# Performance work log

Hardware: AMD Instinct MI355X
Metric: run time of the kernel (lower is better)

Reference implementation:

```python
import jax, jax.numpy as jnp
import numpy as np

B, C, N, M = 4, 256, 4096, 4096
H, D = 4, 64  # num_heads, head_dim = C // H


def _proj(x, W, b):
    # Conv1d(kernel_size=1): pointwise linear over channel dim. x:(B,Cin,L) W:(Cout,Cin) b:(Cout,)
    return jnp.einsum('oc,bcn->bon', W, x) + b[None, :, None]


def setup_inputs() -> dict:
    key = jax.random.key(0)
    ks = jax.random.split(key, 10)
    s = 1.0 / np.sqrt(C)
    return {
        'query': jax.random.normal(ks[0], (B, C, N), dtype=jnp.float32),
        'source': jax.random.normal(ks[1], (B, C, M), dtype=jnp.float32),
        'Wq': jax.random.normal(ks[2], (C, C), dtype=jnp.float32) * s,
        'bq': jnp.zeros((C,), dtype=jnp.float32),
        'Wk': jax.random.normal(ks[3], (C, C), dtype=jnp.float32) * s,
        'bk': jnp.zeros((C,), dtype=jnp.float32),
        'Wv': jax.random.normal(ks[4], (C, C), dtype=jnp.float32) * s,
        'bv': jnp.zeros((C,), dtype=jnp.float32),
        'Wm': jax.random.normal(ks[5], (C, C), dtype=jnp.float32) * s,
        'bm': jnp.zeros((C,), dtype=jnp.float32),
    }


def reference(query, source, Wq, bq, Wk, bk, Wv, bv, Wm, bm):
    b = query.shape[0]
    n = query.shape[-1]
    Q = _proj(query, Wq, bq).reshape(b, H, D, -1)   # (B,H,D,N)
    K = _proj(source, Wk, bk).reshape(b, H, D, -1)  # (B,H,D,M)
    V = _proj(source, Wv, bv).reshape(b, H, D, -1)  # (B,H,D,M)
    scores = jnp.einsum('bhdn,bhdm->bhnm', Q, K) / (D ** 0.5)
    attn = jax.nn.softmax(scores, axis=-1)
    out = jnp.einsum('bhnm,bhdm->bhdn', attn, V)    # (B,H,D,N)
    out = out.reshape(b, H * D, n)                   # (B,C,N)
    return _proj(out, Wm, bm)
```

## Files before the change

kernel.cpp:

```cpp
#include <hip/hip_runtime.h>
#include <hip/hip_bf16.h>
#include <stdint.h>

#define BB 4
#define CCH 256
#define NN 4096
#define MM 4096
#define HH 4
#define DDIM 64

typedef __attribute__((ext_vector_type(8))) short short8v;
typedef __attribute__((ext_vector_type(4))) float f32x4;
typedef __attribute__((ext_vector_type(16))) float f32x16;

__device__ __forceinline__ unsigned short f2b(float f) {
    unsigned int u = __builtin_bit_cast(unsigned int, f);
    unsigned int r = (u + 0x7FFFu + ((u >> 16) & 1u)) >> 16;
    return (unsigned short)r;
}

__device__ __forceinline__ f32x16 zero16() {
    f32x16 z;
#pragma unroll
    for (int i = 0; i < 16; i++) z[i] = 0.f;
    return z;
}

__global__ __launch_bounds__(256) void convert_kernel(
    const float* __restrict__ q, const float* __restrict__ s,
    const float* __restrict__ Wq, const float* __restrict__ Wk,
    const float* __restrict__ Wv, const float* __restrict__ Wm,
    unsigned short* __restrict__ XTq, unsigned short* __restrict__ XTs,
    unsigned short* __restrict__ Wb) {
    __shared__ float tile[64][65];
    const int bid = blockIdx.x, tid = threadIdx.x;
    if (bid < 2048) {
        const float* in = (bid < 1024) ? q : s;
        unsigned short* out = (bid < 1024) ? XTq : XTs;
        const int r = bid & 1023;
        const int b = r >> 8;
        const int rr = r & 255;
        const int l0 = (rr >> 2) * 64, c0 = (rr & 3) * 64;
#pragma unroll
        for (int i = 0; i < 16; i++) {
            int idx = tid + (i << 8);
            int cc = idx >> 6, ll = idx & 63;
            tile[cc][ll] = in[(size_t)(b * CCH + c0 + cc) * 4096 + l0 + ll];
        }
        __syncthreads();
#pragma unroll
        for (int i = 0; i < 16; i++) {
            int idx = tid + (i << 8);
            int ll = idx >> 6, cc = idx & 63;
            out[((size_t)(b * 4096 + l0 + ll) << 8) + c0 + cc] = f2b(tile[cc][ll]);
        }
    } else {
        const int wid = bid - 2048;
        const int wsel = wid >> 4;
        const float* src = (wsel == 0) ? Wq : (wsel == 1) ? Wk : (wsel == 2) ? Wv : Wm;
        const int off = (wid & 15) * 4096;
#pragma unroll
        for (int i = 0; i < 16; i++) {
            int idx = off + tid + (i << 8);
            Wb[(size_t)wsel * 65536 + idx] = f2b(src[idx]);
        }
    }
}

template <int OUTMODE, bool AHEAD>
__device__ __forceinline__ void gemm_body(const unsigned short* __restrict__ XT,
                                          const unsigned short* __restrict__ W,
                                          const float* __restrict__ bias,
                                          void* __restrict__ outv, float oscale) {
    constexpr int WSTR = 264;
    constexpr int XSTR = 40;
    __shared__ __align__(16) unsigned short Wlds[64 * WSTR];
    __shared__ __align__(16) unsigned short Xlds[256 * XSTR];
    const int tid = threadIdx.x, w = tid >> 6, l = tid & 63;
    const int lg = l >> 4, lm = l & 15;
    const int n0 = blockIdx.x * 256, o0 = blockIdx.y * 64;
    const int oh = (w >> 1) * 32, nh = (w & 1) * 128;

#pragma unroll
    for (int i = 0; i < 8; i++) {
        int idx = tid + (i << 8);
        int row = idx >> 5, c8 = (idx & 31) * 8;
        *(uint4*)&Wlds[row * WSTR + c8] = *(const uint4*)&W[(size_t)(o0 + row) * 256 + c8];
    }

    f32x4 acc[8][2];
#pragma unroll
    for (int nt = 0; nt < 8; nt++)
#pragma unroll
        for (int ot = 0; ot < 2; ot++) acc[nt][ot] = (f32x4){0.f, 0.f, 0.f, 0.f};

    for (int kc = 0; kc < 8; kc++) {
#pragma unroll
        for (int i = 0; i < 4; i++) {
            int idx = tid + (i << 8);
            int row = idx >> 2;
            const unsigned short* srcp;
            if constexpr (AHEAD) {
                int c = kc * 32 + (idx & 3) * 8;
                srcp = XT + ((size_t)(c >> 6) * 4096 + n0 + row) * 64 + (c & 63);
            } else {
                srcp = XT + (size_t)(n0 + row) * 256 + kc * 32 + (idx & 3) * 8;
            }
            *(uint4*)&Xlds[row * XSTR + (idx & 3) * 8] = *(const uint4*)srcp;
        }
        __syncthreads();
        short8v bfrag[2];
#pragma unroll
        for (int ot = 0; ot < 2; ot++)
            bfrag[ot] = *(const short8v*)&Wlds[(oh + ot * 16 + lm) * WSTR + kc * 32 + lg * 8];
#pragma unroll
        for (int nt = 0; nt < 8; nt++) {
            short8v af = *(const short8v*)&Xlds[(nh + nt * 16 + lm) * XSTR + lg * 8];
            acc[nt][0] = __builtin_amdgcn_mfma_f32_16x16x32_bf16(af, bfrag[0], acc[nt][0], 0, 0, 0);
            acc[nt][1] = __builtin_amdgcn_mfma_f32_16x16x32_bf16(af, bfrag[1], acc[nt][1], 0, 0, 0);
        }
        __syncthreads();
    }

#pragma unroll
    for (int nt = 0; nt < 8; nt++)
#pragma unroll
        for (int ot = 0; ot < 2; ot++) {
            int o = o0 + oh + ot * 16 + lm;
            int nb = n0 + nh + nt * 16 + lg * 4;
            float bb = bias[o];
            if constexpr (OUTMODE == 2) {
                float* out = (float*)outv;
                float4 v = make_float4(acc[nt][ot][0] + bb, acc[nt][ot][1] + bb,
                                       acc[nt][ot][2] + bb, acc[nt][ot][3] + bb);
                *(float4*)&out[(size_t)o * 4096 + nb] = v;
            } else if constexpr (OUTMODE == 0) {
                unsigned short* out = (unsigned short*)outv;
                __align__(8) unsigned short v[4];
#pragma unroll
                for (int t = 0; t < 4; t++) v[t] = f2b(acc[nt][ot][t] + bb);
                *(uint2*)&out[(size_t)o * 4096 + nb] = *(uint2*)v;
            } else {
                unsigned short* out = (unsigned short*)outv;
                unsigned short* outp = out + ((size_t)(o >> 6) * 4096 + nb) * 64 + (o & 63);
#pragma unroll
                for (int t = 0; t < 4; t++) outp[t * 64] = f2b((acc[nt][ot][t] + bb) * oscale);
            }
        }
}

__global__ __launch_bounds__(256) void gemm_qkv_kernel(
    const unsigned short* __restrict__ XTq, const unsigned short* __restrict__ XTs,
    const unsigned short* __restrict__ Wb,
    const float* __restrict__ bq, const float* __restrict__ bk, const float* __restrict__ bv,
    unsigned short* __restrict__ QT, unsigned short* __restrict__ KT,
    unsigned short* __restrict__ Vn) {
    const int z = blockIdx.z;
    const int b = z / 3, p = z - b * 3;
    const unsigned short* XT = ((p == 0) ? XTq : XTs) + (size_t)b * 4096 * 256;
    const unsigned short* W = Wb + p * 65536;
    const float* bias = (p == 0) ? bq : (p == 1) ? bk : bv;
    if (p == 2) {
        gemm_body<0, false>(XT, W, bias, Vn + (size_t)b * 256 * 4096, 1.0f);
    } else {
        unsigned short* out = ((p == 0) ? QT : KT) + (size_t)b * 1048576;
        gemm_body<1, false>(XT, W, bias, out, (p == 0) ? 0.1803368801f : 1.0f);
    }
}

__global__ __launch_bounds__(256) void gemm_final_kernel(
    const unsigned short* __restrict__ OH, const unsigned short* __restrict__ Wm,
    const float* __restrict__ bm, float* __restrict__ out) {
    const int b = blockIdx.z;
    gemm_body<2, true>(OH + (size_t)b * 1048576, Wm, bm, out + (size_t)b * 256 * 4096, 1.0f);
}

__device__ __forceinline__ void stage_kv(const unsigned short* __restrict__ Kb,
                                         const unsigned short* __restrict__ Vb,
                                         char* dst, int m0s, int tid) {
#pragma unroll
    for (int i = 0; i < 2; i++) {
        int ch = tid + (i << 8);
        int rr = ch >> 3, pp = ch & 7;
        int sw = (pp ^ (rr & 7)) << 4;
        const char* sK = (const char*)(Kb + ((size_t)(m0s + rr) << 6)) + sw;
        const char* sV = (const char*)(Vb + (size_t)rr * 4096 + m0s) + sw;
        __builtin_amdgcn_global_load_lds(
            (const __attribute__((address_space(1))) unsigned int*)sK,
            (__attribute__((address_space(3))) unsigned int*)(dst + (ch << 4)), 16, 0, 0);
        __builtin_amdgcn_global_load_lds(
            (const __attribute__((address_space(1))) unsigned int*)sV,
            (__attribute__((address_space(3))) unsigned int*)(dst + 8192 + (ch << 4)), 16, 0, 0);
    }
}

__global__ __launch_bounds__(256, 2) void attn_kernel(
    const unsigned short* __restrict__ QT, const unsigned short* __restrict__ KT,
    const unsigned short* __restrict__ Vn, unsigned short* __restrict__ OH) {
    __shared__ __align__(16) char smem[32768];
    const int tid = threadIdx.x, w = tid >> 6, l = tid & 63;
    const int lo5 = l & 31, hi = l >> 5;
    const int bh = blockIdx.y, b = bh >> 2, h = bh & 3;
    const int q0 = blockIdx.x * 128 + w * 32;

    short8v qf[4];
    {
        size_t qrow = ((size_t)bh * 4096 + q0 + lo5) * 64;
#pragma unroll
        for (int c = 0; c < 4; c++)
            qf[c] = *(const short8v*)&QT[qrow + c * 16 + hi * 8];
    }

    short8v ones;
#pragma unroll
    for (int j = 0; j < 8; j++) ones[j] = (short)0x3F80;
    f32x16 minit;
#pragma unroll
    for (int r = 0; r < 16; r++) minit[r] = -16.0f;

    const unsigned short* Vb = Vn + ((size_t)b * 256 + h * 64) * 4096;
    const unsigned short* Kb = KT + (size_t)bh * 262144;

    f32x16 o[2];
    o[0] = zero16();
    o[1] = zero16();
    f32x16 sacc = zero16();

    stage_kv(Kb, Vb, smem, 0, tid);

    for (int it = 0; it < 64; it++) {
        __syncthreads();
        char* cur = smem + ((it & 1) << 14);
        if (it < 63) stage_kv(Kb, Vb, smem + (((it + 1) & 1) << 14), (it + 1) * 64, tid);

        short8v kf[2][4];
#pragma unroll
        for (int mc = 0; mc < 2; mc++) {
            int m = mc * 32 + lo5;
#pragma unroll
            for (int c = 0; c < 4; c++)
                kf[mc][c] = *(const short8v*)(cur + m * 128 + (((c * 2 + hi) * 16) ^ ((m & 7) << 4)));
        }
        short8v vf[2][4];
#pragma unroll
        for (int dc = 0; dc < 2; dc++) {
            int d = dc * 32 + lo5;
#pragma unroll
            for (int c = 0; c < 4; c++)
                vf[dc][c] = *(const short8v*)(cur + 8192 + d * 128 + (((c * 2 + hi) * 16) ^ ((d & 7) << 4)));
        }

        f32x16 s[2];
#pragma unroll
        for (int mc = 0; mc < 2; mc++) {
            f32x16 a = __builtin_amdgcn_mfma_f32_32x32x16_bf16(kf[mc][0], qf[0], minit, 0, 0, 0);
#pragma unroll
            for (int c = 1; c < 4; c++)
                a = __builtin_amdgcn_mfma_f32_32x32x16_bf16(kf[mc][c], qf[c], a, 0, 0, 0);
            s[mc] = a;
        }

        short8v pv[2][2];
#pragma unroll
        for (int mc = 0; mc < 2; mc++) {
            float p[16];
#pragma unroll
            for (int r = 0; r < 16; r++) p[r] = exp2f(s[mc][r]);
#pragma unroll
            for (int half = 0; half < 2; half++) {
                union { unsigned int u[4]; short8v v; } pu;
#pragma unroll
                for (int wdx = 0; wdx < 2; wdx++) {
                    unsigned int a, bq;
                    asm("v_cvt_pk_bf16_f32 %0, %1, %2"
                        : "=v"(a) : "v"(p[half * 8 + 2 * wdx]), "v"(p[half * 8 + 2 * wdx + 1]));
                    asm("v_cvt_pk_bf16_f32 %0, %1, %2"
                        : "=v"(bq) : "v"(p[half * 8 + 4 + 2 * wdx]), "v"(p[half * 8 + 4 + 2 * wdx + 1]));
                    asm volatile("v_permlane32_swap_b32 %0, %1" : "+v"(a), "+v"(bq));
                    pu.u[wdx] = a;
                    pu.u[wdx + 2] = bq;
                }
                pv[mc][half] = pu.v;
            }
        }

#pragma unroll
        for (int mc = 0; mc < 2; mc++)
#pragma unroll
            for (int half = 0; half < 2; half++)
                sacc = __builtin_amdgcn_mfma_f32_32x32x16_bf16(ones, pv[mc][half], sacc, 0, 0, 0);

#pragma unroll
        for (int dc = 0; dc < 2; dc++)
#pragma unroll
            for (int mc = 0; mc < 2; mc++)
#pragma unroll
                for (int half = 0; half < 2; half++)
                    o[dc] = __builtin_amdgcn_mfma_f32_32x32x16_bf16(
                        vf[dc][2 * mc + half], pv[mc][half], o[dc], 0, 0, 0);
    }

    float inv = 1.f / sacc[0];
    __syncthreads();
    {
        int row = w * 32 + lo5;
        char* rbase = smem + row * 128;
        int sw = (row & 7) << 4;
#pragma unroll
        for (int dc = 0; dc < 2; dc++)
#pragma unroll
            for (int g = 0; g < 4; g++) {
                ushort4 v4;
                v4.x = f2b(o[dc][g * 4 + 0] * inv);
                v4.y = f2b(o[dc][g * 4 + 1] * inv);
                v4.z = f2b(o[dc][g * 4 + 2] * inv);
                v4.w = f2b(o[dc][g * 4 + 3] * inv);
                int colb = dc * 64 + g * 16 + hi * 8;
                *(ushort4*)(rbase + (colb ^ sw)) = v4;
            }
    }
    __syncthreads();
    {
        int row = tid >> 1, seg = (tid & 1) * 64;
        size_t gbase = ((size_t)bh * 4096 + blockIdx.x * 128 + row) * 64 + (size_t)(tid & 1) * 32;
        int sw = (row & 7) << 4;
#pragma unroll
        for (int ch = 0; ch < 4; ch++) {
            uint4 v = *(const uint4*)(smem + row * 128 + ((seg + ch * 16) ^ sw));
            *(uint4*)&OH[gbase + ch * 8] = v;
        }
    }
}

extern "C" void kernel_launch(void* const* d_in, const int* in_sizes, int n_in,
                              void* d_out, int out_size, void* d_ws, size_t ws_size,
                              hipStream_t stream) {
    const float* q  = (const float*)d_in[0];
    const float* s  = (const float*)d_in[1];
    const float* Wq = (const float*)d_in[2];
    const float* bq = (const float*)d_in[3];
    const float* Wk = (const float*)d_in[4];
    const float* bk = (const float*)d_in[5];
    const float* Wv = (const float*)d_in[6];
    const float* bv = (const float*)d_in[7];
    const float* Wm = (const float*)d_in[8];
    const float* bm = (const float*)d_in[9];
    float* out = (float*)d_out;
    char* ws = (char*)d_ws;

    const size_t SZ = (size_t)BB * 4096 * 256 * 2;
    unsigned short* XTq  = (unsigned short*)(ws);
    unsigned short* XTs  = (unsigned short*)(ws + SZ);
    unsigned short* Wb   = (unsigned short*)(ws + 2 * SZ);
    unsigned short* QT   = (unsigned short*)(ws + 2 * SZ + 524288);
    unsigned short* KTh  = (unsigned short*)(ws + 3 * SZ + 524288);
    unsigned short* Vnat = (unsigned short*)(ws + 4 * SZ + 524288);
    unsigned short* OH   = XTq;

    convert_kernel<<<2112, 256, 0, stream>>>(q, s, Wq, Wk, Wv, Wm, XTq, XTs, Wb);
    gemm_qkv_kernel<<<dim3(16, 4, 12), 256, 0, stream>>>(XTq, XTs, Wb, bq, bk, bv,
                                                         QT, KTh, Vnat);
    attn_kernel<<<dim3(32, 16), 256, 0, stream>>>(QT, KTh, Vnat, OH);
    gemm_final_kernel<<<dim3(16, 4, 4), 256, 0, stream>>>(OH, Wb + 3 * 65536, bm, out);
}
```

Baseline: 228.9 us.

## Triple-buffer K/V staging in attention with explicit vmcnt waits

The attention kernel's K/V LDS staging moves from double to triple buffering, so loads are issued two iterations ahead. Each iteration uses a hand-placed s_waitcnt vmcnt plus a raw s_barrier instead of __syncthreads, so the wait only covers older loads. The goal is to hide more global-to-LDS latency behind the MFMA work. In exchange, LDS per block grows to 48KB, which may limit occupancy, and the kernel now relies on manual wait counts being correct.

```diff
diff --git a/kernel.cpp b/kernel.cpp
--- a/kernel.cpp
+++ b/kernel.cpp
@@ -178,18 +178,22 @@
 __device__ __forceinline__ void stage_kv(const unsigned short* __restrict__ Kb,
                                          const unsigned short* __restrict__ Vb,
                                          char* dst, int m0s, int tid) {
+    const int rr = tid >> 3, pp = tid & 7;
+    const int sw = (pp ^ (rr & 7)) << 4;
+    const char* sK = (const char*)(Kb + ((size_t)(m0s + rr) << 6)) + sw;
+    const char* sV = (const char*)(Vb + (size_t)(rr + 64) * 4096 + m0s - 262144) + sw;
 #pragma unroll
     for (int i = 0; i < 2; i++) {
         int ch = tid + (i << 8);
-        int rr = ch >> 3, pp = ch & 7;
-        int sw = (pp ^ (rr & 7)) << 4;
-        const char* sK = (const char*)(Kb + ((size_t)(m0s + rr) << 6)) + sw;
-        const char* sV = (const char*)(Vb + (size_t)rr * 4096 + m0s) + sw;
+        int r2 = ch >> 3, p2 = ch & 7;
+        int sw2 = (p2 ^ (r2 & 7)) << 4;
+        const char* srcK = (const char*)(Kb + ((size_t)(m0s + r2) << 6)) + sw2;
+        const char* srcV = (const char*)(Vb + (size_t)r2 * 4096 + m0s) + sw2;
         __builtin_amdgcn_global_load_lds(
-            (const __attribute__((address_space(1))) unsigned int*)sK,
+            (const __attribute__((address_space(1))) unsigned int*)srcK,
             (__attribute__((address_space(3))) unsigned int*)(dst + (ch << 4)), 16, 0, 0);
         __builtin_amdgcn_global_load_lds(
-            (const __attribute__((address_space(1))) unsigned int*)sV,
+            (const __attribute__((address_space(1))) unsigned int*)srcV,
             (__attribute__((address_space(3))) unsigned int*)(dst + 8192 + (ch << 4)), 16, 0, 0);
     }
 }
@@ -197,7 +201,7 @@
 __global__ __launch_bounds__(256, 2) void attn_kernel(
     const unsigned short* __restrict__ QT, const unsigned short* __restrict__ KT,
     const unsigned short* __restrict__ Vn, unsigned short* __restrict__ OH) {
-    __shared__ __align__(16) char smem[32768];
+    __shared__ __align__(16) char smem[49152];
     const int tid = threadIdx.x, w = tid >> 6, l = tid & 63;
     const int lo5 = l & 31, hi = l >> 5;
     const int bh = blockIdx.y, b = bh >> 2, h = bh & 3;
@@ -227,11 +231,23 @@
     f32x16 sacc = zero16();
 
     stage_kv(Kb, Vb, smem, 0, tid);
-
+    stage_kv(Kb, Vb, smem + 16384, 64, tid);
+
+    int slot = 0;
     for (int it = 0; it < 64; it++) {
-        __syncthreads();
-        char* cur = smem + ((it & 1) << 14);
-        if (it < 63) stage_kv(Kb, Vb, smem + (((it + 1) & 1) << 14), (it + 1) * 64, tid);
+        if (it == 63)
+            asm volatile("s_waitcnt vmcnt(0)" ::: "memory");
+        else
+            asm volatile("s_waitcnt vmcnt(2)" ::: "memory");
+        __builtin_amdgcn_s_barrier();
+        asm volatile("" ::: "memory");
+
+        char* cur = smem + slot * 16384;
+        if (it < 62) {
+            int ns = slot + 2;
+            if (ns >= 3) ns -= 3;
+            stage_kv(Kb, Vb, smem + ns * 16384, (it + 2) * 64, tid);
+        }
 
         short8v kf[2][4];
 #pragma unroll
@@ -298,6 +314,9 @@
                 for (int half = 0; half < 2; half++)
                     o[dc] = __builtin_amdgcn_mfma_f32_32x32x16_bf16(
                         vf[dc][2 * mc + half], pv[mc][half], o[dc], 0, 0, 0);
+
+        slot++;
+        if (slot == 3) slot = 0;
     }
 
     float inv = 1.f / sacc[0];
```

New measurement: 229.3 us. Within noise of the previous version (+0.2%).
